# Kernel optimization log

Hardware: AMD Instinct MI355X
Metric: run time of the kernel (lower is better)

Reference implementation:

```python
import jax, jax.numpy as jnp
import numpy as np

N = 50000      # nodes
E = 800000     # edges
F_IN = 128     # input node feature dim
H = 4          # attention heads
DH = 64        # per-head hidden dim
HID = H * DH   # 256
NEG_SLOPE = 0.2


def gat_conv(h, src, dst, W, al, ar, b, res):
    # DGL GATConv: project, compute attention logits, edge softmax over dst, aggregate.
    feat = (h @ W).reshape(N, H, DH)                      # [N,H,DH]
    el = jnp.einsum('nhd,hd->nh', feat, al)               # [N,H]
    er = jnp.einsum('nhd,hd->nh', feat, ar)               # [N,H]
    e = el[src] + er[dst]                                 # [E,H]
    e = jnp.where(e > 0, e, NEG_SLOPE * e)                # LeakyReLU(0.2)
    m = jax.ops.segment_max(e, dst, num_segments=N)       # [N,H]
    m = jnp.where(jnp.isfinite(m), m, 0.0)                # zero-in-degree safety
    ex = jnp.exp(e - m[dst])                              # [E,H]
    denom = jax.ops.segment_sum(ex, dst, num_segments=N)  # [N,H]
    alpha = ex / jnp.maximum(denom[dst], 1e-16)           # edge softmax
    out = jax.ops.segment_sum(feat[src] * alpha[:, :, None], dst, num_segments=N)
    return out + res.reshape(N, H, DH) + b.reshape(1, H, DH)


def setup_inputs() -> dict:
    key = jax.random.key(0)
    ks = jax.random.split(key, 16)
    x = jax.random.normal(ks[0], (N, F_IN), jnp.float32)
    edge_index = jax.random.randint(ks[1], (2, E), 0, N)
    s_in = 1.0 / np.sqrt(F_IN)
    s_h = 1.0 / np.sqrt(HID)
    W0 = jax.random.normal(ks[2], (F_IN, HID), jnp.float32) * s_in
    W1 = jax.random.normal(ks[3], (HID, HID), jnp.float32) * s_h
    W2 = jax.random.normal(ks[4], (HID, HID), jnp.float32) * s_h
    al0 = jax.random.normal(ks[5], (H, DH), jnp.float32) * 0.1
    al1 = jax.random.normal(ks[6], (H, DH), jnp.float32) * 0.1
    al2 = jax.random.normal(ks[7], (H, DH), jnp.float32) * 0.1
    ar0 = jax.random.normal(ks[8], (H, DH), jnp.float32) * 0.1
    ar1 = jax.random.normal(ks[9], (H, DH), jnp.float32) * 0.1
    ar2 = jax.random.normal(ks[10], (H, DH), jnp.float32) * 0.1
    b0 = jnp.zeros((HID,), jnp.float32)
    b1 = jnp.zeros((HID,), jnp.float32)
    b2 = jnp.zeros((HID,), jnp.float32)
    resW0 = jax.random.normal(ks[11], (F_IN, HID), jnp.float32) * s_in
    return {"x": x, "edge_index": edge_index,
            "W0": W0, "W1": W1, "W2": W2,
            "al0": al0, "al1": al1, "al2": al2,
            "ar0": ar0, "ar1": ar1, "ar2": ar2,
            "b0": b0, "b1": b1, "b2": b2,
            "resW0": resW0}


def reference(x, edge_index, W0, W1, W2, al0, al1, al2, ar0, ar1, ar2, b0, b1, b2, resW0):
    src, dst = edge_index[0], edge_index[1]
    # layer 0: residual via linear projection (in != heads*hidden)
    h = gat_conv(x, src, dst, W0, al0, ar0, b0, x @ resW0).reshape(N, HID)
    h = jax.nn.relu(h)
    # layer 1: identity residual
    h = gat_conv(h, src, dst, W1, al1, ar1, b1, h).reshape(N, HID)
    h = jax.nn.relu(h)
    # layer 2: identity residual, mean over heads
    h = gat_conv(h, src, dst, W2, al2, ar2, b2, h)
    return h.mean(axis=1)  # [N, DH]
```

## Files before the change

kernel.cpp:

```cpp
#include <hip/hip_runtime.h>
#include <math.h>

#define N_NODES 50000
#define N_EDGES 800000
#define F_INPUT 128
#define HEADS 4
#define DHID 64
#define HID 256
#define M_PAD 50048
#define SCAN_B 49

typedef _Float16 half8 __attribute__((ext_vector_type(8)));
typedef _Float16 half4 __attribute__((ext_vector_type(4)));
typedef float f32x4 __attribute__((ext_vector_type(4)));


__global__ void hist_kernel(const int* __restrict__ dst, int* __restrict__ counts) {
    int e = blockIdx.x * 256 + threadIdx.x;
    if (e < N_EDGES) atomicAdd(&counts[dst[e]], 1);
}

__global__ __launch_bounds__(256) void scan1_kernel(const int* __restrict__ counts,
                                                    int* __restrict__ pre,
                                                    int* __restrict__ bsum) {
    __shared__ int buf[256];
    int tid = threadIdx.x;
    int idx = blockIdx.x * 1024 + tid * 4;
    int v0 = 0, v1 = 0, v2 = 0, v3 = 0;
    if (idx + 3 < N_NODES) {
        int4 v = *(const int4*)&counts[idx];
        v0 = v.x; v1 = v.y; v2 = v.z; v3 = v.w;
    } else {
        if (idx + 0 < N_NODES) v0 = counts[idx + 0];
        if (idx + 1 < N_NODES) v1 = counts[idx + 1];
        if (idx + 2 < N_NODES) v2 = counts[idx + 2];
    }
    int s0 = v0, s1 = s0 + v1, s2 = s1 + v2, s3 = s2 + v3;
    buf[tid] = s3;
    __syncthreads();
    for (int off = 1; off < 256; off <<= 1) {
        int t = (tid >= off) ? buf[tid - off] : 0;
        __syncthreads();
        buf[tid] += t;
        __syncthreads();
    }
    int excl = buf[tid] - s3;
    if (idx + 0 < N_NODES) pre[idx + 0] = excl + s0;
    if (idx + 1 < N_NODES) pre[idx + 1] = excl + s1;
    if (idx + 2 < N_NODES) pre[idx + 2] = excl + s2;
    if (idx + 3 < N_NODES) pre[idx + 3] = excl + s3;
    if (tid == 255) bsum[blockIdx.x] = buf[255];
}

__global__ void scan2_kernel(const int* __restrict__ bsum, int* __restrict__ bpre) {
    int lane = threadIdx.x;
    int v = (lane < SCAN_B) ? bsum[lane] : 0;
    int orig = v;
#pragma unroll
    for (int off = 1; off < 64; off <<= 1) {
        int t = __shfl_up(v, off, 64);
        if (lane >= off) v += t;
    }
    if (lane < SCAN_B) bpre[lane] = v - orig;
}

__global__ __launch_bounds__(256) void scan3_kernel(const int* __restrict__ pre,
                                                    const int* __restrict__ bpre,
                                                    int* __restrict__ row_ptr) {
    int add = bpre[blockIdx.x];
    int idx = blockIdx.x * 1024 + threadIdx.x * 4;
#pragma unroll
    for (int u = 0; u < 4; u++) {
        int i = idx + u;
        if (i < N_NODES) row_ptr[i + 1] = pre[i] + add;
    }
    if (blockIdx.x == 0 && threadIdx.x == 0) row_ptr[0] = 0;
}

__global__ void scatter_kernel(const int* __restrict__ src, const int* __restrict__ dst,
                               const int* __restrict__ row_ptr, int* __restrict__ cursor,
                               int* __restrict__ esrc) {
    int e = blockIdx.x * 256 + threadIdx.x;
    if (e < N_EDGES) {
        int d = dst[e];
        int pos = row_ptr[d] + atomicAdd(&cursor[d], 1);
        esrc[pos] = src[e];
    }
}


__global__ void cvt_x_kernel(const float* __restrict__ x, _Float16* __restrict__ x16) {
    int t = blockIdx.x * 256 + threadIdx.x;
    if (t < N_NODES * F_INPUT / 4) {
        f32x4 v = *(const f32x4*)&x[t * 4];
        half4 h = {(_Float16)v.x, (_Float16)v.y, (_Float16)v.z, (_Float16)v.w};
        *(half4*)&x16[(size_t)t * 4] = h;
    }
}

__global__ void wt_all_kernel(const float* __restrict__ W0, const float* __restrict__ WR,
                              _Float16* __restrict__ WtL0,
                              const float* __restrict__ W1, _Float16* __restrict__ Wt1,
                              const float* __restrict__ W2, _Float16* __restrict__ Wt2) {
    int t = blockIdx.x * 256 + threadIdx.x;
    if (t < 65536) {
        int c = t >> 7;
        int k = t & 127;
        float v = (c < 256) ? W0[k * 256 + c] : WR[k * 256 + (c - 256)];
        WtL0[t] = (_Float16)v;
    } else if (t < 131072) {
        int u = t - 65536;
        int c = u >> 8;
        int k = u & 255;
        Wt1[u] = (_Float16)W1[k * 256 + c];
    } else if (t < 196608) {
        int u = t - 131072;
        int c = u >> 8;
        int k = u & 255;
        Wt2[u] = (_Float16)W2[k * 256 + c];
    }
}


__device__ __forceinline__ void gl2lds16(const void* g, void* l) {
    __builtin_amdgcn_global_load_lds((const __attribute__((address_space(1))) void*)g,
                                     (__attribute__((address_space(3))) void*)l, 16, 0, 0);
}

__global__ __launch_bounds__(512) void gemm_l0(const _Float16* __restrict__ A16,
                                               const _Float16* __restrict__ WtL0,
                                               _Float16* __restrict__ feat16,
                                               float* __restrict__ res32,
                                               const float* __restrict__ al,
                                               const float* __restrict__ ar,
                                               float* __restrict__ el, float* __restrict__ er) {
    __shared__ __align__(16) _Float16 As[4 * 512];
    __shared__ __align__(16) _Float16 Ws[32 * 512];
    int tid = threadIdx.x;
    int w = tid >> 6;
    int lane = tid & 63;
    int lrow = lane & 15;
    int lk = lane >> 4;
    int row0 = blockIdx.x * 64;

    f32x4 acc[4][4] = {};

    for (int k0 = 0; k0 < F_INPUT; k0 += 32) {
        if (w < 4)
            gl2lds16(A16 + (size_t)(row0 + w * 16 + lrow) * F_INPUT + k0 + lk * 8, &As[w * 512]);
#pragma unroll
        for (int i = 0; i < 4; i++) {
            int tt = i * 8 + w;
            gl2lds16(WtL0 + (size_t)(tt * 16 + lrow) * F_INPUT + k0 + lk * 8, &Ws[tt * 512]);
        }
        __syncthreads();
        half8 a[4], b[4];
#pragma unroll
        for (int m = 0; m < 4; m++) a[m] = *(const half8*)&As[m * 512 + lane * 8];
#pragma unroll
        for (int j = 0; j < 4; j++) b[j] = *(const half8*)&Ws[(w * 4 + j) * 512 + lane * 8];
#pragma unroll
        for (int m = 0; m < 4; m++)
#pragma unroll
            for (int j = 0; j < 4; j++)
                acc[m][j] = __builtin_amdgcn_mfma_f32_16x16x32_f16(a[m], b[j], acc[m][j], 0, 0, 0);
        __syncthreads();
    }

    if (w < 4) {
        float alv[4], arv[4];
#pragma unroll
        for (int j = 0; j < 4; j++) {
            alv[j] = al[w * 64 + j * 16 + lrow];
            arv[j] = ar[w * 64 + j * 16 + lrow];
        }
#pragma unroll
        for (int m = 0; m < 4; m++) {
#pragma unroll
            for (int r = 0; r < 4; r++) {
                int row = row0 + m * 16 + lk * 4 + r;
                if (row < N_NODES) {
#pragma unroll
                    for (int j = 0; j < 4; j++)
                        feat16[(size_t)row * HID + w * 64 + j * 16 + lrow] = (_Float16)acc[m][j][r];
                }
                float pl = acc[m][0][r] * alv[0] + acc[m][1][r] * alv[1] +
                           acc[m][2][r] * alv[2] + acc[m][3][r] * alv[3];
                float pr = acc[m][0][r] * arv[0] + acc[m][1][r] * arv[1] +
                           acc[m][2][r] * arv[2] + acc[m][3][r] * arv[3];
#pragma unroll
                for (int off = 1; off < 16; off <<= 1) {
                    pl += __shfl_xor(pl, off, 64);
                    pr += __shfl_xor(pr, off, 64);
                }
                if (lrow == 0 && row < N_NODES) {
                    el[row * 4 + w] = pl;
                    er[row * 4 + w] = pr;
                }
            }
        }
    } else {
        int wc = w - 4;
#pragma unroll
        for (int m = 0; m < 4; m++) {
#pragma unroll
            for (int r = 0; r < 4; r++) {
                int row = row0 + m * 16 + lk * 4 + r;
                if (row < N_NODES) {
#pragma unroll
                    for (int j = 0; j < 4; j++)
                        res32[(size_t)row * HID + wc * 64 + j * 16 + lrow] = acc[m][j][r];
                }
            }
        }
    }
}

__global__ __launch_bounds__(512) void gemm_h(const _Float16* __restrict__ A16,
                                              const _Float16* __restrict__ Wt,
                                              _Float16* __restrict__ feat16,
                                              const float* __restrict__ al,
                                              const float* __restrict__ ar,
                                              float* __restrict__ el, float* __restrict__ er) {
    __shared__ __align__(16) _Float16 As[8 * 512];
    __shared__ __align__(16) _Float16 Ws[16 * 512];
    int tid = threadIdx.x;
    int w = tid >> 6;
    int lane = tid & 63;
    int lrow = lane & 15;
    int lk = lane >> 4;
    int wrow = w >> 2;
    int wcol = w & 3;
    int row0 = blockIdx.x * 128;

    f32x4 acc[4][4] = {};

    for (int k0 = 0; k0 < HID; k0 += 32) {
        gl2lds16(A16 + (size_t)(row0 + w * 16 + lrow) * HID + k0 + lk * 8, &As[w * 512]);
        gl2lds16(Wt + (size_t)(w * 16 + lrow) * HID + k0 + lk * 8, &Ws[w * 512]);
        gl2lds16(Wt + (size_t)((w + 8) * 16 + lrow) * HID + k0 + lk * 8, &Ws[(w + 8) * 512]);
        __syncthreads();
        half8 a[4], b[4];
#pragma unroll
        for (int m = 0; m < 4; m++) a[m] = *(const half8*)&As[(wrow * 4 + m) * 512 + lane * 8];
#pragma unroll
        for (int j = 0; j < 4; j++) b[j] = *(const half8*)&Ws[(wcol * 4 + j) * 512 + lane * 8];
#pragma unroll
        for (int m = 0; m < 4; m++)
#pragma unroll
            for (int j = 0; j < 4; j++)
                acc[m][j] = __builtin_amdgcn_mfma_f32_16x16x32_f16(a[m], b[j], acc[m][j], 0, 0, 0);
        __syncthreads();
    }

    float alv[4], arv[4];
#pragma unroll
    for (int j = 0; j < 4; j++) {
        alv[j] = al[wcol * 64 + j * 16 + lrow];
        arv[j] = ar[wcol * 64 + j * 16 + lrow];
    }
#pragma unroll
    for (int m = 0; m < 4; m++) {
#pragma unroll
        for (int r = 0; r < 4; r++) {
            int row = row0 + wrow * 64 + m * 16 + lk * 4 + r;
            if (row < N_NODES) {
#pragma unroll
                for (int j = 0; j < 4; j++)
                    feat16[(size_t)row * HID + wcol * 64 + j * 16 + lrow] = (_Float16)acc[m][j][r];
            }
            float pl = acc[m][0][r] * alv[0] + acc[m][1][r] * alv[1] +
                       acc[m][2][r] * alv[2] + acc[m][3][r] * alv[3];
            float pr = acc[m][0][r] * arv[0] + acc[m][1][r] * arv[1] +
                       acc[m][2][r] * arv[2] + acc[m][3][r] * arv[3];
#pragma unroll
            for (int off = 1; off < 16; off <<= 1) {
                pl += __shfl_xor(pl, off, 64);
                pr += __shfl_xor(pr, off, 64);
            }
            if (lrow == 0 && row < N_NODES) {
                el[row * 4 + wcol] = pl;
                er[row * 4 + wcol] = pr;
            }
        }
    }
}


__global__ __launch_bounds__(256) void agg_kernel(const _Float16* __restrict__ feat16,
                                                  const float* __restrict__ el,
                                                  const float* __restrict__ er,
                                                  const int* __restrict__ row_ptr,
                                                  const int* __restrict__ esrc,
                                                  const float* __restrict__ res,
                                                  const float* __restrict__ bias,
                                                  float* __restrict__ out32,
                                                  _Float16* __restrict__ out16,
                                                  float* __restrict__ outmean,
                                                  int do_relu) {
    __shared__ float lds[4][64 * 5];
    int wv = threadIdx.x >> 6;
    int lane = threadIdx.x & 63;
    int n = blockIdx.x * 4 + wv;
    int head = lane >> 4;
    int start = row_ptr[n];
    int deg = row_ptr[n + 1] - start;
    f32x4 ern = *(const f32x4*)&er[n * 4];
    float* L = lds[wv];

    f32x4 acc = {0.f, 0.f, 0.f, 0.f};
    float smh = 0.f;

    if (deg <= 64) {
        int s = 0;
        f32x4 x = {-1e30f, -1e30f, -1e30f, -1e30f};
        if (lane < deg) {
            s = esrc[start + lane];
            f32x4 v = *(const f32x4*)&el[s * 4];
            v = v + ern;
            x.x = v.x > 0.f ? v.x : 0.2f * v.x;
            x.y = v.y > 0.f ? v.y : 0.2f * v.y;
            x.z = v.z > 0.f ? v.z : 0.2f * v.z;
            x.w = v.w > 0.f ? v.w : 0.2f * v.w;
        }
        f32x4 cm = x;
#pragma unroll
        for (int off = 1; off < 64; off <<= 1) {
            cm.x = fmaxf(cm.x, __shfl_xor(cm.x, off, 64));
            cm.y = fmaxf(cm.y, __shfl_xor(cm.y, off, 64));
            cm.z = fmaxf(cm.z, __shfl_xor(cm.z, off, 64));
            cm.w = fmaxf(cm.w, __shfl_xor(cm.w, off, 64));
        }
        f32x4 ex4;
        ex4.x = __expf(x.x - cm.x);
        ex4.y = __expf(x.y - cm.y);
        ex4.z = __expf(x.z - cm.z);
        ex4.w = __expf(x.w - cm.w);
        L[lane * 5 + 0] = ex4.x;
        L[lane * 5 + 1] = ex4.y;
        L[lane * 5 + 2] = ex4.z;
        L[lane * 5 + 3] = ex4.w;
        L[lane * 5 + 4] = __int_as_float(s);
        f32x4 cs = ex4;
#pragma unroll
        for (int off = 1; off < 64; off <<= 1) {
            cs.x += __shfl_xor(cs.x, off, 64);
            cs.y += __shfl_xor(cs.y, off, 64);
            cs.z += __shfl_xor(cs.z, off, 64);
            cs.w += __shfl_xor(cs.w, off, 64);
        }
        smh = (head == 0) ? cs.x : (head == 1) ? cs.y : (head == 2) ? cs.z : cs.w;

        int j = 0;
        for (; j + 4 <= deg; j += 4) {
            float exv[4]; int ssv[4];
#pragma unroll
            for (int u = 0; u < 4; u++) {
                exv[u] = L[(j + u) * 5 + head];
                ssv[u] = __float_as_int(L[(j + u) * 5 + 4]);
            }
            half4 f[4];
#pragma unroll
            for (int u = 0; u < 4; u++)
                f[u] = *(const half4*)&feat16[(size_t)ssv[u] * HID + lane * 4];
#pragma unroll
            for (int u = 0; u < 4; u++) {
                acc.x += exv[u] * (float)f[u].x;
                acc.y += exv[u] * (float)f[u].y;
                acc.z += exv[u] * (float)f[u].z;
                acc.w += exv[u] * (float)f[u].w;
            }
        }
        for (; j < deg; j++) {
            float ex = L[j * 5 + head];
            int ss = __float_as_int(L[j * 5 + 4]);
            half4 f = *(const half4*)&feat16[(size_t)ss * HID + lane * 4];
            acc.x += ex * (float)f.x;
            acc.y += ex * (float)f.y;
            acc.z += ex * (float)f.z;
            acc.w += ex * (float)f.w;
        }
    } else {
        f32x4 mx = {-1e30f, -1e30f, -1e30f, -1e30f};
        for (int base = 0; base < deg; base += 64) {
            int e = base + lane;
            int s = 0;
            f32x4 x = {-1e30f, -1e30f, -1e30f, -1e30f};
            if (e < deg) {
                s = esrc[start + e];
                f32x4 v = *(const f32x4*)&el[s * 4];
                v = v + ern;
                x.x = v.x > 0.f ? v.x : 0.2f * v.x;
                x.y = v.y > 0.f ? v.y : 0.2f * v.y;
                x.z = v.z > 0.f ? v.z : 0.2f * v.z;
                x.w = v.w > 0.f ? v.w : 0.2f * v.w;
            }
            f32x4 cm = x;
#pragma unroll
            for (int off = 1; off < 64; off <<= 1) {
                cm.x = fmaxf(cm.x, __shfl_xor(cm.x, off, 64));
                cm.y = fmaxf(cm.y, __shfl_xor(cm.y, off, 64));
                cm.z = fmaxf(cm.z, __shfl_xor(cm.z, off, 64));
                cm.w = fmaxf(cm.w, __shfl_xor(cm.w, off, 64));
            }
            f32x4 nmx;
            nmx.x = fmaxf(mx.x, cm.x);
            nmx.y = fmaxf(mx.y, cm.y);
            nmx.z = fmaxf(mx.z, cm.z);
            nmx.w = fmaxf(mx.w, cm.w);
            float mxh  = (head == 0) ? mx.x  : (head == 1) ? mx.y  : (head == 2) ? mx.z  : mx.w;
            float nmxh = (head == 0) ? nmx.x : (head == 1) ? nmx.y : (head == 2) ? nmx.z : nmx.w;
            float sc = __expf(mxh - nmxh);
            smh *= sc;
            acc = acc * sc;
            f32x4 ex4;
            ex4.x = __expf(x.x - nmx.x);
            ex4.y = __expf(x.y - nmx.y);
            ex4.z = __expf(x.z - nmx.z);
            ex4.w = __expf(x.w - nmx.w);
            L[lane * 5 + 0] = ex4.x;
            L[lane * 5 + 1] = ex4.y;
            L[lane * 5 + 2] = ex4.z;
            L[lane * 5 + 3] = ex4.w;
            L[lane * 5 + 4] = __int_as_float(s);
            f32x4 cs = ex4;
#pragma unroll
            for (int off = 1; off < 64; off <<= 1) {
                cs.x += __shfl_xor(cs.x, off, 64);
                cs.y += __shfl_xor(cs.y, off, 64);
                cs.z += __shfl_xor(cs.z, off, 64);
                cs.w += __shfl_xor(cs.w, off, 64);
            }
            smh += (head == 0) ? cs.x : (head == 1) ? cs.y : (head == 2) ? cs.z : cs.w;

            int cnt = min(64, deg - base);
            int j = 0;
            for (; j + 4 <= cnt; j += 4) {
                float exv[4]; int ssv[4];
#pragma unroll
                for (int u = 0; u < 4; u++) {
                    exv[u] = L[(j + u) * 5 + head];
                    ssv[u] = __float_as_int(L[(j + u) * 5 + 4]);
                }
                half4 f[4];
#pragma unroll
                for (int u = 0; u < 4; u++)
                    f[u] = *(const half4*)&feat16[(size_t)ssv[u] * HID + lane * 4];
#pragma unroll
                for (int u = 0; u < 4; u++) {
                    acc.x += exv[u] * (float)f[u].x;
                    acc.y += exv[u] * (float)f[u].y;
                    acc.z += exv[u] * (float)f[u].z;
                    acc.w += exv[u] * (float)f[u].w;
                }
            }
            for (; j < cnt; j++) {
                float ex = L[j * 5 + head];
                int ss = __float_as_int(L[j * 5 + 4]);
                half4 f = *(const half4*)&feat16[(size_t)ss * HID + lane * 4];
                acc.x += ex * (float)f.x;
                acc.y += ex * (float)f.y;
                acc.z += ex * (float)f.z;
                acc.w += ex * (float)f.w;
            }
            mx = nmx;
        }
    }

    float inv = 1.f / fmaxf(smh, 1e-16f);
    f32x4 o = acc * inv;
    o = o + *(const f32x4*)&res[(size_t)n * HID + lane * 4] + *(const f32x4*)&bias[lane * 4];
    if (do_relu) {
        o.x = fmaxf(o.x, 0.f);
        o.y = fmaxf(o.y, 0.f);
        o.z = fmaxf(o.z, 0.f);
        o.w = fmaxf(o.w, 0.f);
    }
    if (outmean) {
        o.x += __shfl_xor(o.x, 16, 64); o.x += __shfl_xor(o.x, 32, 64);
        o.y += __shfl_xor(o.y, 16, 64); o.y += __shfl_xor(o.y, 32, 64);
        o.z += __shfl_xor(o.z, 16, 64); o.z += __shfl_xor(o.z, 32, 64);
        o.w += __shfl_xor(o.w, 16, 64); o.w += __shfl_xor(o.w, 32, 64);
        if (head == 0) {
            f32x4 mo = o * 0.25f;
            *(f32x4*)&outmean[(size_t)n * DHID + (lane & 15) * 4] = mo;
        }
    } else {
        *(f32x4*)&out32[(size_t)n * HID + lane * 4] = o;
        half4 h = {(_Float16)o.x, (_Float16)o.y, (_Float16)o.z, (_Float16)o.w};
        *(half4*)&out16[(size_t)n * HID + lane * 4] = h;
    }
}


extern "C" void kernel_launch(void* const* d_in, const int* in_sizes, int n_in,
                              void* d_out, int out_size, void* d_ws, size_t ws_size,
                              hipStream_t stream) {
    const float* x     = (const float*)d_in[0];
    const int*   ei    = (const int*)d_in[1];
    const float* W0    = (const float*)d_in[2];
    const float* W1    = (const float*)d_in[3];
    const float* W2    = (const float*)d_in[4];
    const float* al0   = (const float*)d_in[5];
    const float* al1   = (const float*)d_in[6];
    const float* al2   = (const float*)d_in[7];
    const float* ar0   = (const float*)d_in[8];
    const float* ar1   = (const float*)d_in[9];
    const float* ar2   = (const float*)d_in[10];
    const float* b0    = (const float*)d_in[11];
    const float* b1    = (const float*)d_in[12];
    const float* b2    = (const float*)d_in[13];
    const float* resW0 = (const float*)d_in[14];
    float* out = (float*)d_out;

    const int* srcp = ei;
    const int* dstp = ei + N_EDGES;

    char* p = (char*)d_ws;
    auto alloc = [&](size_t bytes) -> char* {
        char* r = p;
        p += (bytes + 255) & ~(size_t)255;
        return r;
    };
    float*     H32    = (float*)alloc((size_t)N_NODES * HID * 4);
    _Float16*  H16    = (_Float16*)alloc((size_t)M_PAD * HID * 2);
    _Float16*  feat16 = (_Float16*)alloc((size_t)M_PAD * HID * 2);
    _Float16*  x16    = (_Float16*)alloc((size_t)M_PAD * F_INPUT * 2);
    float*     el     = (float*)alloc((size_t)N_NODES * HEADS * 4);
    float*     er     = (float*)alloc((size_t)N_NODES * HEADS * 4);
    _Float16*  WtL0   = (_Float16*)alloc((size_t)512 * F_INPUT * 2);
    _Float16*  Wt1    = (_Float16*)alloc((size_t)HID * HID * 2);
    _Float16*  Wt2    = (_Float16*)alloc((size_t)HID * HID * 2);
    int*       counts = (int*)alloc((size_t)2 * N_NODES * 4);
    int*       cursor = counts + N_NODES;
    int*       rowptr = (int*)alloc((size_t)(N_NODES + 1) * 4);
    int*       esrc   = (int*)alloc((size_t)N_EDGES * 4);
    int*       pre    = (int*)alloc((size_t)N_NODES * 4);
    int*       bsum   = (int*)alloc((size_t)SCAN_B * 4);
    int*       bpre   = (int*)alloc((size_t)SCAN_B * 4);

    const int EB = (N_EDGES + 255) / 256;
    const int NB = N_NODES / 4;

    hipMemsetAsync(counts, 0, (size_t)2 * N_NODES * 4, stream);
    hist_kernel<<<EB, 256, 0, stream>>>(dstp, counts);
    scan1_kernel<<<SCAN_B, 256, 0, stream>>>(counts, pre, bsum);
    scan2_kernel<<<1, 64, 0, stream>>>(bsum, bpre);
    scan3_kernel<<<SCAN_B, 256, 0, stream>>>(pre, bpre, rowptr);
    scatter_kernel<<<EB, 256, 0, stream>>>(srcp, dstp, rowptr, cursor, esrc);

    cvt_x_kernel<<<(N_NODES * F_INPUT / 4 + 255) / 256, 256, 0, stream>>>(x, x16);
    wt_all_kernel<<<768, 256, 0, stream>>>(W0, resW0, WtL0, W1, Wt1, W2, Wt2);

    gemm_l0<<<M_PAD / 64, 512, 0, stream>>>(x16, WtL0, feat16, H32, al0, ar0, el, er);
    agg_kernel<<<NB, 256, 0, stream>>>(feat16, el, er, rowptr, esrc, H32, b0, H32, H16, nullptr, 1);

    gemm_h<<<M_PAD / 128, 512, 0, stream>>>(H16, Wt1, feat16, al1, ar1, el, er);
    agg_kernel<<<NB, 256, 0, stream>>>(feat16, el, er, rowptr, esrc, H32, b1, H32, H16, nullptr, 1);

    gemm_h<<<M_PAD / 128, 512, 0, stream>>>(H16, Wt2, feat16, al2, ar2, el, er);
    agg_kernel<<<NB, 256, 0, stream>>>(feat16, el, er, rowptr, esrc, H32, b2, nullptr, nullptr, out, 0);
}
```

Before: 517.9 us.

## Fold attention vectors into weight matrix and store residual activations in fp16

```diff
diff --git a/kernel.cpp b/kernel.cpp
--- a/kernel.cpp
+++ b/kernel.cpp
@@ -121,6 +121,51 @@
     }
 }
 
+__global__ void wlwr_kernel(const float* __restrict__ W0, const float* __restrict__ al0,
+                            const float* __restrict__ ar0, _Float16* __restrict__ WtL0,
+                            const float* __restrict__ W1, const float* __restrict__ al1,
+                            const float* __restrict__ ar1, _Float16* __restrict__ Wt1,
+                            const float* __restrict__ W2, const float* __restrict__ al2,
+                            const float* __restrict__ ar2, _Float16* __restrict__ Wt2) {
+    int t = blockIdx.x * 256 + threadIdx.x;
+    if (t < 2048) {
+        int row8 = t >> 7, k = t & 127;
+        float v = 0.f;
+        if (row8 < 8) {
+            int h = row8 & 3;
+            const float* vec = (row8 < 4) ? al0 : ar0;
+            float s = 0.f;
+            for (int d = 0; d < 64; d++) s += W0[k * 256 + h * 64 + d] * vec[h * 64 + d];
+            v = s;
+        }
+        WtL0[(512 + row8) * 128 + k] = (_Float16)v;
+    } else if (t < 6144) {
+        int u = t - 2048;
+        int row8 = u >> 8, k = u & 255;
+        float v = 0.f;
+        if (row8 < 8) {
+            int h = row8 & 3;
+            const float* vec = (row8 < 4) ? al1 : ar1;
+            float s = 0.f;
+            for (int d = 0; d < 64; d++) s += W1[k * 256 + h * 64 + d] * vec[h * 64 + d];
+            v = s;
+        }
+        Wt1[(256 + row8) * 256 + k] = (_Float16)v;
+    } else if (t < 10240) {
+        int u = t - 6144;
+        int row8 = u >> 8, k = u & 255;
+        float v = 0.f;
+        if (row8 < 8) {
+            int h = row8 & 3;
+            const float* vec = (row8 < 4) ? al2 : ar2;
+            float s = 0.f;
+            for (int d = 0; d < 64; d++) s += W2[k * 256 + h * 64 + d] * vec[h * 64 + d];
+            v = s;
+        }
+        Wt2[(256 + row8) * 256 + k] = (_Float16)v;
+    }
+}
+
 
 __device__ __forceinline__ void gl2lds16(const void* g, void* l) {
     __builtin_amdgcn_global_load_lds((const __attribute__((address_space(1))) void*)g,
@@ -130,12 +175,10 @@
 __global__ __launch_bounds__(512) void gemm_l0(const _Float16* __restrict__ A16,
                                                const _Float16* __restrict__ WtL0,
                                                _Float16* __restrict__ feat16,
-                                               float* __restrict__ res32,
-                                               const float* __restrict__ al,
-                                               const float* __restrict__ ar,
+                                               _Float16* __restrict__ res16,
                                                float* __restrict__ el, float* __restrict__ er) {
     __shared__ __align__(16) _Float16 As[4 * 512];
-    __shared__ __align__(16) _Float16 Ws[32 * 512];
+    __shared__ __align__(16) _Float16 Ws[33 * 512];
     int tid = threadIdx.x;
     int w = tid >> 6;
     int lane = tid & 63;
@@ -144,6 +187,7 @@
     int row0 = blockIdx.x * 64;
 
     f32x4 acc[4][4] = {};
+    f32x4 acc5[4] = {};
 
     for (int k0 = 0; k0 < F_INPUT; k0 += 32) {
         if (w < 4)
@@ -153,27 +197,29 @@
             int tt = i * 8 + w;
             gl2lds16(WtL0 + (size_t)(tt * 16 + lrow) * F_INPUT + k0 + lk * 8, &Ws[tt * 512]);
         }
+        if (w == 7)
+            gl2lds16(WtL0 + (size_t)(512 + lrow) * F_INPUT + k0 + lk * 8, &Ws[32 * 512]);
         __syncthreads();
-        half8 a[4], b[4];
+        half8 a[4], b[4], b5;
 #pragma unroll
         for (int m = 0; m < 4; m++) a[m] = *(const half8*)&As[m * 512 + lane * 8];
 #pragma unroll
         for (int j = 0; j < 4; j++) b[j] = *(const half8*)&Ws[(w * 4 + j) * 512 + lane * 8];
+        if (w == 3) b5 = *(const half8*)&Ws[32 * 512 + lane * 8];
 #pragma unroll
         for (int m = 0; m < 4; m++)
 #pragma unroll
             for (int j = 0; j < 4; j++)
                 acc[m][j] = __builtin_amdgcn_mfma_f32_16x16x32_f16(a[m], b[j], acc[m][j], 0, 0, 0);
+        if (w == 3) {
+#pragma unroll
+            for (int m = 0; m < 4; m++)
+                acc5[m] = __builtin_amdgcn_mfma_f32_16x16x32_f16(a[m], b5, acc5[m], 0, 0, 0);
+        }
         __syncthreads();
     }
 
     if (w < 4) {
-        float alv[4], arv[4];
-#pragma unroll
-        for (int j = 0; j < 4; j++) {
-            alv[j] = al[w * 64 + j * 16 + lrow];
-            arv[j] = ar[w * 64 + j * 16 + lrow];
-        }
 #pragma unroll
         for (int m = 0; m < 4; m++) {
 #pragma unroll
@@ -184,18 +230,19 @@
                     for (int j = 0; j < 4; j++)
                         feat16[(size_t)row * HID + w * 64 + j * 16 + lrow] = (_Float16)acc[m][j][r];
                 }
-                float pl = acc[m][0][r] * alv[0] + acc[m][1][r] * alv[1] +
-                           acc[m][2][r] * alv[2] + acc[m][3][r] * alv[3];
-                float pr = acc[m][0][r] * arv[0] + acc[m][1][r] * arv[1] +
-                           acc[m][2][r] * arv[2] + acc[m][3][r] * arv[3];
-#pragma unroll
-                for (int off = 1; off < 16; off <<= 1) {
-                    pl += __shfl_xor(pl, off, 64);
-                    pr += __shfl_xor(pr, off, 64);
-                }
-                if (lrow == 0 && row < N_NODES) {
-                    el[row * 4 + w] = pl;
-                    er[row * 4 + w] = pr;
+            }
+        }
+        if (w == 3 && lrow < 8) {
+#pragma unroll
+            for (int m = 0; m < 4; m++) {
+#pragma unroll
+                for (int r = 0; r < 4; r++) {
+                    int row = row0 + m * 16 + lk * 4 + r;
+                    if (row < N_NODES) {
+                        float v = acc5[m][r];
+                        if (lrow < 4) el[row * 4 + lrow] = v;
+                        else          er[row * 4 + (lrow - 4)] = v;
+                    }
                 }
             }
         }
@@ -209,7 +256,7 @@
                 if (row < N_NODES) {
 #pragma unroll
                     for (int j = 0; j < 4; j++)
-                        res32[(size_t)row * HID + wc * 64 + j * 16 + lrow] = acc[m][j][r];
+                        res16[(size_t)row * HID + wc * 64 + j * 16 + lrow] = (_Float16)acc[m][j][r];
                 }
             }
         }
@@ -219,11 +266,9 @@
 __global__ __launch_bounds__(512) void gemm_h(const _Float16* __restrict__ A16,
                                               const _Float16* __restrict__ Wt,
                                               _Float16* __restrict__ feat16,
-                                              const float* __restrict__ al,
-                                              const float* __restrict__ ar,
                                               float* __restrict__ el, float* __restrict__ er) {
     __shared__ __align__(16) _Float16 As[8 * 512];
-    __shared__ __align__(16) _Float16 Ws[16 * 512];
+    __shared__ __align__(16) _Float16 Ws[17 * 512];
     int tid = threadIdx.x;
     int w = tid >> 6;
     int lane = tid & 63;
@@ -234,31 +279,34 @@
     int row0 = blockIdx.x * 128;
 
     f32x4 acc[4][4] = {};
+    f32x4 acc5[4] = {};
 
     for (int k0 = 0; k0 < HID; k0 += 32) {
         gl2lds16(A16 + (size_t)(row0 + w * 16 + lrow) * HID + k0 + lk * 8, &As[w * 512]);
         gl2lds16(Wt + (size_t)(w * 16 + lrow) * HID + k0 + lk * 8, &Ws[w * 512]);
         gl2lds16(Wt + (size_t)((w + 8) * 16 + lrow) * HID + k0 + lk * 8, &Ws[(w + 8) * 512]);
+        if (w == 0)
+            gl2lds16(Wt + (size_t)(256 + lrow) * HID + k0 + lk * 8, &Ws[16 * 512]);
         __syncthreads();
-        half8 a[4], b[4];
+        half8 a[4], b[4], b5;
 #pragma unroll
         for (int m = 0; m < 4; m++) a[m] = *(const half8*)&As[(wrow * 4 + m) * 512 + lane * 8];
 #pragma unroll
         for (int j = 0; j < 4; j++) b[j] = *(const half8*)&Ws[(wcol * 4 + j) * 512 + lane * 8];
+        if (wcol == 3) b5 = *(const half8*)&Ws[16 * 512 + lane * 8];
 #pragma unroll
         for (int m = 0; m < 4; m++)
 #pragma unroll
             for (int j = 0; j < 4; j++)
                 acc[m][j] = __builtin_amdgcn_mfma_f32_16x16x32_f16(a[m], b[j], acc[m][j], 0, 0, 0);
+        if (wcol == 3) {
+#pragma unroll
+            for (int m = 0; m < 4; m++)
+                acc5[m] = __builtin_amdgcn_mfma_f32_16x16x32_f16(a[m], b5, acc5[m], 0, 0, 0);
+        }
         __syncthreads();
     }
 
-    float alv[4], arv[4];
-#pragma unroll
-    for (int j = 0; j < 4; j++) {
-        alv[j] = al[wcol * 64 + j * 16 + lrow];
-        arv[j] = ar[wcol * 64 + j * 16 + lrow];
-    }
 #pragma unroll
     for (int m = 0; m < 4; m++) {
 #pragma unroll
@@ -269,18 +317,19 @@
                 for (int j = 0; j < 4; j++)
                     feat16[(size_t)row * HID + wcol * 64 + j * 16 + lrow] = (_Float16)acc[m][j][r];
             }
-            float pl = acc[m][0][r] * alv[0] + acc[m][1][r] * alv[1] +
-                       acc[m][2][r] * alv[2] + acc[m][3][r] * alv[3];
-            float pr = acc[m][0][r] * arv[0] + acc[m][1][r] * arv[1] +
-                       acc[m][2][r] * arv[2] + acc[m][3][r] * arv[3];
-#pragma unroll
-            for (int off = 1; off < 16; off <<= 1) {
-                pl += __shfl_xor(pl, off, 64);
-                pr += __shfl_xor(pr, off, 64);
-            }
-            if (lrow == 0 && row < N_NODES) {
-                el[row * 4 + wcol] = pl;
-                er[row * 4 + wcol] = pr;
+        }
+    }
+    if (wcol == 3 && lrow < 8) {
+#pragma unroll
+        for (int m = 0; m < 4; m++) {
+#pragma unroll
+            for (int r = 0; r < 4; r++) {
+                int row = row0 + wrow * 64 + m * 16 + lk * 4 + r;
+                if (row < N_NODES) {
+                    float v = acc5[m][r];
+                    if (lrow < 4) el[row * 4 + lrow] = v;
+                    else          er[row * 4 + (lrow - 4)] = v;
+                }
             }
         }
     }
@@ -292,9 +341,8 @@
                                                   const float* __restrict__ er,
                                                   const int* __restrict__ row_ptr,
                                                   const int* __restrict__ esrc,
-                                                  const float* __restrict__ res,
+                                                  const _Float16* __restrict__ res16,
                                                   const float* __restrict__ bias,
-                                                  float* __restrict__ out32,
                                                   _Float16* __restrict__ out16,
                                                   float* __restrict__ outmean,
                                                   int do_relu) {
@@ -469,7 +517,12 @@
 
     float inv = 1.f / fmaxf(smh, 1e-16f);
     f32x4 o = acc * inv;
-    o = o + *(const f32x4*)&res[(size_t)n * HID + lane * 4] + *(const f32x4*)&bias[lane * 4];
+    half4 rv = *(const half4*)&res16[(size_t)n * HID + lane * 4];
+    f32x4 bv = *(const f32x4*)&bias[lane * 4];
+    o.x += (float)rv.x + bv.x;
+    o.y += (float)rv.y + bv.y;
+    o.z += (float)rv.z + bv.z;
+    o.w += (float)rv.w + bv.w;
     if (do_relu) {
         o.x = fmaxf(o.x, 0.f);
         o.y = fmaxf(o.y, 0.f);
@@ -486,7 +539,6 @@
             *(f32x4*)&outmean[(size_t)n * DHID + (lane & 15) * 4] = mo;
         }
     } else {
-        *(f32x4*)&out32[(size_t)n * HID + lane * 4] = o;
         half4 h = {(_Float16)o.x, (_Float16)o.y, (_Float16)o.z, (_Float16)o.w};
         *(half4*)&out16[(size_t)n * HID + lane * 4] = h;
     }
@@ -522,15 +574,15 @@
         p += (bytes + 255) & ~(size_t)255;
         return r;
     };
-    float*     H32    = (float*)alloc((size_t)N_NODES * HID * 4);
-    _Float16*  H16    = (_Float16*)alloc((size_t)M_PAD * HID * 2);
+    _Float16*  h16    = (_Float16*)alloc((size_t)M_PAD * HID * 2);
     _Float16*  feat16 = (_Float16*)alloc((size_t)M_PAD * HID * 2);
+    _Float16*  res0   = (_Float16*)alloc((size_t)N_NODES * HID * 2);
     _Float16*  x16    = (_Float16*)alloc((size_t)M_PAD * F_INPUT * 2);
     float*     el     = (float*)alloc((size_t)N_NODES * HEADS * 4);
     float*     er     = (float*)alloc((size_t)N_NODES * HEADS * 4);
-    _Float16*  WtL0   = (_Float16*)alloc((size_t)512 * F_INPUT * 2);
-    _Float16*  Wt1    = (_Float16*)alloc((size_t)HID * HID * 2);
-    _Float16*  Wt2    = (_Float16*)alloc((size_t)HID * HID * 2);
+    _Float16*  WtL0   = (_Float16*)alloc((size_t)528 * F_INPUT * 2);
+    _Float16*  Wt1    = (_Float16*)alloc((size_t)272 * HID * 2);
+    _Float16*  Wt2    = (_Float16*)alloc((size_t)272 * HID * 2);
     int*       counts = (int*)alloc((size_t)2 * N_NODES * 4);
     int*       cursor = counts + N_NODES;
     int*       rowptr = (int*)alloc((size_t)(N_NODES + 1) * 4);
@@ -551,13 +603,14 @@
 
     cvt_x_kernel<<<(N_NODES * F_INPUT / 4 + 255) / 256, 256, 0, stream>>>(x, x16);
     wt_all_kernel<<<768, 256, 0, stream>>>(W0, resW0, WtL0, W1, Wt1, W2, Wt2);
-
-    gemm_l0<<<M_PAD / 64, 512, 0, stream>>>(x16, WtL0, feat16, H32, al0, ar0, el, er);
-    agg_kernel<<<NB, 256, 0, stream>>>(feat16, el, er, rowptr, esrc, H32, b0, H32, H16, nullptr, 1);
-
-    gemm_h<<<M_PAD / 128, 512, 0, stream>>>(H16, Wt1, feat16, al1, ar1, el, er);
-    agg_kernel<<<NB, 256, 0, stream>>>(feat16, el, er, rowptr, esrc, H32, b1, H32, H16, nullptr, 1);
-
-    gemm_h<<<M_PAD / 128, 512, 0, stream>>>(H16, Wt2, feat16, al2, ar2, el, er);
-    agg_kernel<<<NB, 256, 0, stream>>>(feat16, el, er, rowptr, esrc, H32, b2, nullptr, nullptr, out, 0);
-}
+    wlwr_kernel<<<40, 256, 0, stream>>>(W0, al0, ar0, WtL0, W1, al1, ar1, Wt1, W2, al2, ar2, Wt2);
+
+    gemm_l0<<<M_PAD / 64, 512, 0, stream>>>(x16, WtL0, feat16, res0, el, er);
+    agg_kernel<<<NB, 256, 0, stream>>>(feat16, el, er, rowptr, esrc, res0, b0, h16, nullptr, 1);
+
+    gemm_h<<<M_PAD / 128, 512, 0, stream>>>(h16, Wt1, feat16, el, er);
+    agg_kernel<<<NB, 256, 0, stream>>>(feat16, el, er, rowptr, esrc, h16, b1, h16, nullptr, 1);
+
+    gemm_h<<<M_PAD / 128, 512, 0, stream>>>(h16, Wt2, feat16, el, er);
+    agg_kernel<<<NB, 256, 0, stream>>>(feat16, el, er, rowptr, esrc, h16, b2, nullptr, out, 0);
+}
```

Measured after the change: 494.3 us. -4.6%, faster.
